# Kernel tuning notes

Measured on AMD Instinct MI355X. Metric: run time of the kernel, lower is better.

The kernel has to match this reference:

```python
import jax, jax.numpy as jnp
import numpy as np

NUM_CAPSULE = 5
DIM_CAPSULE = 5
ROUTINGS = 4
T_EPSILON = 1e-07


def squash(x, axis=-1):
    # Note: this module's 'squash' is pure norm-normalization (no v^2/(1+v^2) factor)
    s_squared_norm = jnp.sum(x * x, axis=axis, keepdims=True)
    return x / jnp.sqrt(s_squared_norm + T_EPSILON)


def setup_inputs() -> dict:
    key = jax.random.key(0)
    k1, k2 = jax.random.split(key)
    batch, seq, d_in = 1024, 512, 120
    x = jax.random.normal(k1, (batch, seq, d_in), dtype=jnp.float32)
    # xavier_normal for fan_in=120, fan_out=25
    std = float(np.sqrt(2.0 / (d_in + NUM_CAPSULE * DIM_CAPSULE)))
    W = jax.random.normal(k2, (1, d_in, NUM_CAPSULE * DIM_CAPSULE), dtype=jnp.float32) * std
    return {"x": x, "W": W}


def reference(x, W):
    batch, inp, _ = x.shape
    # u_hat_vecs: [batch, num_capsule, input_num_capsule, dim_capsule]
    u_hat = jnp.matmul(x, W[0])  # [b, inp, 25]
    u_hat = u_hat.reshape(batch, inp, NUM_CAPSULE, DIM_CAPSULE).transpose(0, 2, 1, 3)
    b = jnp.zeros((batch, NUM_CAPSULE, inp), dtype=u_hat.dtype)
    outputs = None
    for i in range(ROUTINGS):
        # torch code softmaxes over the num_capsule axis (dim 1 of b)
        c = jax.nn.softmax(b, axis=1)  # [b, ncaps, inp]
        outputs = squash(jnp.einsum('bij,bijk->bik', c, u_hat))  # [b, ncaps, dcap]
        if i < ROUTINGS - 1:
            b = jnp.einsum('bik,bijk->bij', outputs, u_hat)
    return outputs
```

## Files before the change

kernel.cpp:

```cpp
#include <hip/hip_runtime.h>


#define NCAP 5
#define DCAP 5
#define NOUT 25
#define DIN 120
#define SEQ 512
#define ROUTINGS 4

__global__ __launch_bounds__(256) void gemm_kernel(
    const float* __restrict__ x,
    const float* __restrict__ W,
    float* __restrict__ uh)
{
    const int gid = blockIdx.x * 256 + threadIdx.x;
    const int b   = gid >> 9;
    const int r   = gid & 511;
    const float* xr = x + (size_t)gid * DIN;

    float acc[NOUT];
#pragma unroll
    for (int j = 0; j < NOUT; ++j) acc[j] = 0.f;

#pragma unroll 1
    for (int ch = 0; ch < 6; ++ch) {
        float4 v[5];
#pragma unroll
        for (int u = 0; u < 5; ++u)
            v[u] = *(const float4*)(xr + ch * 20 + 4 * u);
#pragma unroll
        for (int u = 0; u < 5; ++u) {
            const float* wr = W + (ch * 20 + 4 * u) * NOUT;
#pragma unroll
            for (int j = 0; j < NOUT; ++j) {
                float w0 = wr[j];
                float w1 = wr[j + NOUT];
                float w2 = wr[j + 2 * NOUT];
                float w3 = wr[j + 3 * NOUT];
                acc[j] = fmaf(v[u].w, w3,
                         fmaf(v[u].z, w2,
                         fmaf(v[u].y, w1,
                         fmaf(v[u].x, w0, acc[j]))));
            }
        }
    }

    float* ub = uh + (size_t)b * NOUT * SEQ + r;
#pragma unroll
    for (int j = 0; j < NOUT; ++j) ub[(size_t)j * SEQ] = acc[j];
}

__global__ __launch_bounds__(256) void route_kernel(
    const float* __restrict__ uh,
    float* __restrict__ out)
{
    const int b    = blockIdx.x;
    const int t    = threadIdx.x;
    const int lane = t & 63;
    const int wv   = t >> 6;

    __shared__ float red[4][NOUT];

    const float* ub = uh + (size_t)b * NOUT * SEQ;
    float u0[NOUT], u1[NOUT];
#pragma unroll
    for (int j = 0; j < NOUT; ++j) {
        u0[j] = ub[(size_t)j * SEQ + t];
        u1[j] = ub[(size_t)j * SEQ + t + 256];
    }

    float bb0[NCAP], bb1[NCAP];
#pragma unroll
    for (int c = 0; c < NCAP; ++c) { bb0[c] = 0.f; bb1[c] = 0.f; }

    float s[NOUT], sc[NCAP];

    for (int it = 0; it < ROUTINGS; ++it) {
        float m0 = bb0[0], m1 = bb1[0];
#pragma unroll
        for (int c = 1; c < NCAP; ++c) { m0 = fmaxf(m0, bb0[c]); m1 = fmaxf(m1, bb1[c]); }
        float e0[NCAP], e1[NCAP]; float se0 = 0.f, se1 = 0.f;
#pragma unroll
        for (int c = 0; c < NCAP; ++c) {
            e0[c] = __expf(bb0[c] - m0); se0 += e0[c];
            e1[c] = __expf(bb1[c] - m1); se1 += e1[c];
        }
        float i0 = 1.f / se0, i1 = 1.f / se1;

        float p[NOUT];
#pragma unroll
        for (int c = 0; c < NCAP; ++c) {
            float c0 = e0[c] * i0, c1 = e1[c] * i1;
#pragma unroll
            for (int k = 0; k < DCAP; ++k)
                p[c*DCAP + k] = fmaf(c0, u0[c*DCAP + k], c1 * u1[c*DCAP + k]);
        }

#pragma unroll
        for (int d = 1; d < 64; d <<= 1)
#pragma unroll
            for (int j = 0; j < NOUT; ++j) p[j] += __shfl_xor(p[j], d, 64);

        if (lane == 0) {
#pragma unroll
            for (int j = 0; j < NOUT; ++j) red[wv][j] = p[j];
        }
        __syncthreads();
#pragma unroll
        for (int j = 0; j < NOUT; ++j)
            s[j] = red[0][j] + red[1][j] + red[2][j] + red[3][j];
        __syncthreads();

#pragma unroll
        for (int c = 0; c < NCAP; ++c) {
            float ss = 0.f;
#pragma unroll
            for (int k = 0; k < DCAP; ++k)
                ss = fmaf(s[c*DCAP + k], s[c*DCAP + k], ss);
            sc[c] = rsqrtf(ss + 1e-7f);
        }

        if (it < ROUTINGS - 1) {
#pragma unroll
            for (int c = 0; c < NCAP; ++c) {
                float d0 = 0.f, d1 = 0.f;
#pragma unroll
                for (int k = 0; k < DCAP; ++k) {
                    float oc = s[c*DCAP + k] * sc[c];
                    d0 = fmaf(oc, u0[c*DCAP + k], d0);
                    d1 = fmaf(oc, u1[c*DCAP + k], d1);
                }
                bb0[c] = d0; bb1[c] = d1;
            }
        }
    }

    if (t < NOUT) out[(size_t)b * NOUT + t] = s[t] * sc[t / DCAP];
}

extern "C" void kernel_launch(void* const* d_in, const int* in_sizes, int n_in,
                              void* d_out, int out_size, void* d_ws, size_t ws_size,
                              hipStream_t stream) {
    const float* x   = (const float*)d_in[0];
    const float* W   = (const float*)d_in[1];
    float*       o   = (float*)d_out;
    float*       uh  = (float*)d_ws;
    const int batch  = in_sizes[0] / (SEQ * DIN);

    gemm_kernel<<<dim3(batch * 2), dim3(256), 0, stream>>>(x, W, uh);
    route_kernel<<<dim3(batch),    dim3(256), 0, stream>>>(uh, o);
}
```

Baseline: 465.6 us.

## Stage x tiles into LDS with async global_load_lds double buffering

```diff
diff --git a/kernel.cpp b/kernel.cpp
--- a/kernel.cpp
+++ b/kernel.cpp
@@ -8,44 +8,76 @@
 #define SEQ 512
 #define ROUTINGS 4
 
+#define KT    12
+#define NTILE 10
+#define RPB   256
+#define BUFF  (RPB * KT)
+
+typedef __attribute__((address_space(3))) void        as3_void;
+typedef const __attribute__((address_space(1))) void  as1_void;
+
 __global__ __launch_bounds__(256) void gemm_kernel(
     const float* __restrict__ x,
     const float* __restrict__ W,
     float* __restrict__ uh)
 {
-    const int gid = blockIdx.x * 256 + threadIdx.x;
-    const int b   = gid >> 9;
-    const int r   = gid & 511;
-    const float* xr = x + (size_t)gid * DIN;
+    const int blk  = blockIdx.x;
+    const int b    = blk >> 1;
+    const int half = blk & 1;
+    const int t    = threadIdx.x;
+    const int wv   = t >> 6;
+
+    __shared__ float xt[2][BUFF];
+
+    const float* xb = x + ((size_t)b * SEQ + half * RPB) * DIN;
+
+    auto stage = [&](int bufi, int tile) {
+        const int k0 = tile * KT;
+#pragma unroll
+        for (int i = 0; i < 3; ++i) {
+            unsigned f   = (unsigned)t + 256u * (unsigned)i;
+            unsigned row = f / 3u;
+            unsigned q   = f - row * 3u;
+            const float* gsrc = xb + row * DIN + k0 + 4u * q;
+            float*      ldst = &xt[bufi][1024 * i + 256 * wv];
+            __builtin_amdgcn_global_load_lds((as1_void*)gsrc, (as3_void*)ldst,
+                                             16, 0, 0);
+        }
+    };
 
     float acc[NOUT];
 #pragma unroll
     for (int j = 0; j < NOUT; ++j) acc[j] = 0.f;
 
-#pragma unroll 1
-    for (int ch = 0; ch < 6; ++ch) {
-        float4 v[5];
+    stage(0, 0);
+    __syncthreads();
+
+    for (int tile = 0; tile < NTILE; ++tile) {
+        const int cur = tile & 1;
+        if (tile + 1 < NTILE) stage(cur ^ 1, tile + 1);
+
+        const int k0 = tile * KT;
+        const float* r0 = &xt[cur][t * KT];
 #pragma unroll
-        for (int u = 0; u < 5; ++u)
-            v[u] = *(const float4*)(xr + ch * 20 + 4 * u);
-#pragma unroll
-        for (int u = 0; u < 5; ++u) {
-            const float* wr = W + (ch * 20 + 4 * u) * NOUT;
+        for (int q = 0; q < 3; ++q) {
+            float4 a = *(const float4*)(r0 + 4 * q);
+            const float* wr = W + (k0 + 4 * q) * NOUT;
 #pragma unroll
             for (int j = 0; j < NOUT; ++j) {
                 float w0 = wr[j];
                 float w1 = wr[j + NOUT];
                 float w2 = wr[j + 2 * NOUT];
                 float w3 = wr[j + 3 * NOUT];
-                acc[j] = fmaf(v[u].w, w3,
-                         fmaf(v[u].z, w2,
-                         fmaf(v[u].y, w1,
-                         fmaf(v[u].x, w0, acc[j]))));
+                acc[j] = fmaf(a.w, w3,
+                         fmaf(a.z, w2,
+                         fmaf(a.y, w1,
+                         fmaf(a.x, w0, acc[j]))));
             }
         }
+        __syncthreads();
     }
 
-    float* ub = uh + (size_t)b * NOUT * SEQ + r;
+    float* ub = uh + (size_t)b * NOUT * SEQ + half * RPB + t;
 #pragma unroll
     for (int j = 0; j < NOUT; ++j) ub[(size_t)j * SEQ] = acc[j];
 }
```

After: 421.2 us. 9.5% less time.
